# Kernel tuning notes

Measured on AMD Instinct MI355X. Metric: run time of the kernel, lower is better.

Reference implementation:

```python
import jax, jax.numpy as jnp
import numpy as np
from jax import lax

CODEBOOK_DIM = 32
SCALE_SCHEDULE = [1, 2, 4, 8, 16, 32, 64, 128, 256, 512, 1024, 2048, 4096, 8192]
INV_TEMP = 100.0
COMMIT_W = 0.2
ENTROPY_W = 0.1
EPS_NORM = 1e-12
EPS_LOG = 1e-8


def setup_inputs() -> dict:
    key = jax.random.key(0)
    B, T, C = 32, 8192, CODEBOOK_DIM
    f_BTC = jax.random.normal(key, (B, T, C), dtype=jnp.float32)
    return {"f_BTC": f_BTC}


def _area_down(x, pt):
    # torch F.interpolate mode='area' on divisible sizes == average pooling
    B, T, C = x.shape
    if pt == T:
        return x
    return x.reshape(B, pt, T // pt, C).mean(axis=2)


def _linear_up(x, out_size):
    # torch F.interpolate mode='linear', align_corners=False
    B, in_size, C = x.shape
    if out_size == in_size:
        return x
    scale = in_size / out_size
    pos = (jnp.arange(out_size, dtype=jnp.float32) + 0.5) * scale - 0.5
    pos = jnp.clip(pos, 0.0, in_size - 1)
    lo = jnp.floor(pos).astype(jnp.int32)
    hi = jnp.minimum(lo + 1, in_size - 1)
    w = (pos - lo.astype(jnp.float32))[None, :, None]
    return x[:, lo] * (1.0 - w) + x[:, hi] * w


def _bsq_level(z):
    # normalize
    norm = jnp.sqrt(jnp.sum(z * z, axis=-1, keepdims=True))
    z = z / jnp.maximum(norm, EPS_NORM)
    q_scale = 1.0 / (CODEBOOK_DIM ** 0.5)
    zhat = jnp.where(z > 0, q_scale, -q_scale).astype(z.dtype)
    quant = z + lax.stop_gradient(zhat - z)  # STE
    # soft entropy loss
    p = jax.nn.sigmoid(-4.0 * z / (CODEBOOK_DIM ** 0.5) * INV_TEMP)
    ent = lambda c: -(c * jnp.log(c + EPS_LOG))
    per_sample = (ent(p) + ent(1.0 - p)).sum(axis=-1).mean()
    avg_p = p.mean(axis=(0, 1))  # [C]
    cb_ent = (ent(avg_p) + ent(1.0 - avg_p)).sum()
    entropy_penalty = (per_sample - cb_ent) / INV_TEMP
    commit = jnp.mean(((lax.stop_gradient(quant) - z) ** 2).sum(axis=-1))
    aux = entropy_penalty * ENTROPY_W + commit * COMMIT_W
    bits = (quant > 0).astype(jnp.int32)
    return quant, bits, aux


def reference(f_BTC):
    B, T, C = f_BTC.shape
    quantized_out = jnp.zeros_like(f_BTC)
    residual = f_BTC
    all_losses, all_bits = [], []
    for pt in SCALE_SCHEDULE:
        r = _area_down(residual, pt)
        quant, bits, loss = _bsq_level(r)
        q_up = _linear_up(quant, T)
        residual = residual - lax.stop_gradient(q_up)
        quantized_out = quantized_out + q_up
        all_bits.append(bits)
        all_losses.append(loss)
    return quantized_out, jnp.concatenate(all_bits, axis=1), jnp.stack(all_losses, axis=-1)
```

## Files before the change

kernel.cpp:

```cpp
#include <hip/hip_runtime.h>

#define B_DIM 32
#define T_DIM 8192
#define C_DIM 32
#define N_ELEM (B_DIM * T_DIM * C_DIM)
#define SUM_PT 16383
#define BITS_ELEM (B_DIM * SUM_PT * C_DIM)
#define NLEVEL 14
#define PARTW 2048
#define QSCALE 0.17677669529663687f
#define ALPHA  70.710678118654755f

#define OWN 128
#define HALO 16
#define MAXL (OWN + 2 * HALO)

__device__ __forceinline__ float entf(float x) { return -(x * __logf(x + 1e-8f)); }
__device__ __forceinline__ float qval(float bit) { return bit * (2.0f * QSCALE) - QSCALE; }

__device__ __forceinline__ float interp_pk(const unsigned int* __restrict__ pkbase,
                                           int ptj, float tpos, int c) {
    const float a = (float)ptj * (1.0f / (float)T_DIM);
    float pos = (tpos + 0.5f) * a - 0.5f;
    pos = fminf(fmaxf(pos, 0.0f), (float)(ptj - 1));
    const int lo = (int)pos;
    const int hi = min(lo + 1, ptj - 1);
    const float w = pos - (float)lo;
    const float b0 = (float)((pkbase[lo] >> c) & 1u);
    const float b1 = (float)((pkbase[hi] >> c) & 1u);
    return ((b0 * (1.0f - w) + b1 * w) * 2.0f - 1.0f) * QSCALE;
}

template <int PTJ>
__device__ __forceinline__ float interp_loc(const unsigned int* __restrict__ bl,
                                            int p0, float tpos, int c) {
    const float a = (float)PTJ * (1.0f / (float)T_DIM);
    float pos = (tpos + 0.5f) * a - 0.5f;
    pos = fminf(fmaxf(pos, 0.0f), (float)(PTJ - 1));
    const int lo = (int)pos;
    const int hi = min(lo + 1, PTJ - 1);
    const float w = pos - (float)lo;
    const float b0 = (float)((bl[lo - p0] >> c) & 1u);
    const float b1 = (float)((bl[hi - p0] >> c) & 1u);
    return ((b0 * (1.0f - w) + b1 * w) * 2.0f - 1.0f) * QSCALE;
}

__device__ float pooled_up_sum64(const float* base, int ptj, int m) {
    const int W = 64;
    const float a = (float)ptj * (1.0f / (float)T_DIM);
    const float p0 = ((float)(m * W) + 0.5f) * a - 0.5f;
    const float pmax = (float)(ptj - 1);
    float sum = 0.0f;
    int iL = 0;
    if (p0 < 0.0f) { iL = (int)ceilf(-p0 / a); if (iL > W) iL = W; }
    int iH = W - 1;
    if (p0 + (float)(W - 1) * a > pmax) {
        iH = (int)floorf((pmax - p0) / a);
        if (iH > W - 1) iH = W - 1;
        if (iH < -1) iH = -1;
    }
    if (iL > 0) sum += (float)iL * qval(base[0]);
    if (iH < W - 1) sum += (float)(W - 1 - iH) * qval(base[(size_t)(ptj - 1) * C_DIM]);
    if (iH >= iL) {
        const float pL = p0 + (float)iL * a;
        int l0 = (int)pL;
        if (l0 > ptj - 1) l0 = ptj - 1;
        const int is = (int)ceilf(((float)(l0 + 1) - p0) / a);
        const int endA = min(is - 1, iH);
        if (endA >= iL) {
            const int nA = endA - iL + 1;
            const float sI = 0.5f * (float)(iL + endA) * (float)nA;
            const float SA = (float)nA * (p0 - (float)l0) + a * sI;
            const float q0 = qval(base[(size_t)l0 * C_DIM]);
            const float q1 = qval(base[(size_t)min(l0 + 1, ptj - 1) * C_DIM]);
            sum += (float)nA * q0 + SA * (q1 - q0);
        }
        const int begB = max(is, iL);
        if (begB <= iH) {
            const int nB = iH - begB + 1;
            const float sI = 0.5f * (float)(begB + iH) * (float)nB;
            const float SB = (float)nB * (p0 - (float)(l0 + 1)) + a * sI;
            const float q1 = qval(base[(size_t)min(l0 + 1, ptj - 1) * C_DIM]);
            const float q2 = qval(base[(size_t)min(l0 + 2, ptj - 1) * C_DIM]);
            sum += (float)nB * q1 + SB * (q2 - q1);
        }
    }
    return sum;
}

template <int NT>
__device__ __forceinline__ void write_partials(float eAcc, float cAcc, float pAcc,
                                               float* partial, int level, int col) {
    __shared__ float sP[NT];
    __shared__ float sEC[NT / 16];
    __syncthreads();
    const int grp = threadIdx.x >> 5, c = threadIdx.x & 31;
    float eg = eAcc, cg = cAcc;
#pragma unroll
    for (int m = 16; m >= 1; m >>= 1) { eg += __shfl_xor(eg, m, 32); cg += __shfl_xor(cg, m, 32); }
    if (c == 0) { sEC[grp * 2] = eg; sEC[grp * 2 + 1] = cg; }
    sP[threadIdx.x] = pAcc;
    __syncthreads();
    float* base = partial + (size_t)level * 34 * PARTW;
    if (threadIdx.x < 32) {
        float ps = 0.f;
#pragma unroll
        for (int r = 0; r < NT / 32; ++r) ps += sP[threadIdx.x + r * 32];
        base[(size_t)(2 + threadIdx.x) * PARTW + col] = ps;
    }
    if (threadIdx.x == 0) {
        float se = 0.f, sc = 0.f;
#pragma unroll
        for (int g = 0; g < NT / 32; ++g) { se += sEC[2 * g]; sc += sEC[2 * g + 1]; }
        base[0 * PARTW + col] = se;
        base[(size_t)1 * PARTW + col] = sc;
    }
}

__device__ __forceinline__ float bsq_eval(float v, float& bit, float& pA, float& eA, float& cA) {
    float sq = v * v;
#pragma unroll
    for (int m = 16; m >= 1; m >>= 1) sq += __shfl_xor(sq, m, 32);
    const float z = v / fmaxf(sqrtf(sq), 1e-12f);
    bit = (z > 0.f) ? 1.0f : 0.0f;
    const float zh = (z > 0.f) ? QSCALE : -QSCALE;
    const float d = zh - z;
    cA += d * d;
    const float p = 1.0f / (1.0f + __expf(ALPHA * z));
    pA += p;
    eA += entf(p) + entf(1.0f - p);
    return zh;
}

__global__ void init_kernel(const float* __restrict__ f, float* __restrict__ F128) {
    const int b = blockIdx.x >> 7, m = blockIdx.x & 127;
    const int c = threadIdx.x & 31, grp = threadIdx.x >> 5;
    const float* fb = f + ((size_t)b * T_DIM + m * 64 + grp * 8) * C_DIM + c;
    float s = 0.f;
#pragma unroll
    for (int i = 0; i < 8; ++i) s += fb[i * C_DIM];
    __shared__ float red[8][32];
    red[grp][c] = s;
    __syncthreads();
    if (grp == 0) {
        float t = red[0][c] + red[1][c] + red[2][c] + red[3][c]
                + red[4][c] + red[5][c] + red[6][c] + red[7][c];
        F128[((size_t)b * 128 + m) * C_DIM + c] = t * (1.0f / 64.0f);
    }
}

__global__ __launch_bounds__(1024) void fused_small_kernel(const float* __restrict__ F128,
                                                           float* __restrict__ bits,
                                                           unsigned int* __restrict__ pkG,
                                                           float* __restrict__ partial) {
    const int b = blockIdx.x;
    __shared__ float P[128 * 32];
    __shared__ float qh[127 * 32];
    const int c = threadIdx.x & 31, grp = threadIdx.x >> 5;
    for (int i = threadIdx.x; i < 128 * 32; i += 1024) P[i] = F128[(size_t)b * 128 * 32 + i];
    __syncthreads();
    for (int k = 0; k < 8; ++k) {
        const int pt = 1 << k, W2 = 128 >> k;
        float pAcc = 0.f, eAcc = 0.f, cAcc = 0.f;
        for (int o = grp; o < pt; o += 32) {
            float v = 0.f;
            for (int i = 0; i < W2; ++i) v += P[(o * W2 + i) * 32 + c];
            v *= (1.0f / (float)W2);
            float bit;
            bsq_eval(v, bit, pAcc, eAcc, cAcc);
            bits[((size_t)b * SUM_PT + (pt - 1) + o) * C_DIM + c] = bit;
            const unsigned long long bal = __ballot(bit > 0.5f);
            if (c == 0)
                pkG[(size_t)b * 256 + (pt - 1) + o] =
                    (threadIdx.x & 32) ? (unsigned)(bal >> 32) : (unsigned)bal;
            if (k < 7) qh[((pt - 1) + o) * 32 + c] = bit;
        }
        write_partials<1024>(eAcc, cAcc, pAcc, partial, k, b);
        if (k < 7) {
            __syncthreads();
            for (int m = grp; m < 128; m += 32)
                P[m * 32 + c] -= pooled_up_sum64(&qh[(pt - 1) * 32 + c], 1 << k, m) * (1.0f / 64.0f);
            __syncthreads();
        }
    }
}

template <int K, int OFF>
__device__ __forceinline__ void cf_level(float* Rl, unsigned int* bitsPyr,
                                         const float* wT, const int* iT,
                                         float* __restrict__ bits,
                                         float* __restrict__ partial, int b,
                                         int L0, int nL, int r0, int r1,
                                         int c, int grp) {
    constexpr int F = 4096 >> K;
    constexpr int ptk = 1 << K;
    const int p0 = L0 / F, pN = nL / F;
    const int own0 = r0 / F, own1 = r1 / F;
    unsigned int* bl = bitsPyr + OFF;
    float pAcc = 0.f, eAcc = 0.f, cAcc = 0.f;
    for (int pl = grp; pl < pN; pl += 16) {
        float v = 0.f;
#pragma unroll
        for (int r = 0; r < F; ++r) v += Rl[(pl * F + r) * 32 + c];
        v *= (1.0f / (float)F);
        float sq = v * v;
#pragma unroll
        for (int m = 16; m >= 1; m >>= 1) sq += __shfl_xor(sq, m, 32);
        const float z = v / fmaxf(sqrtf(sq), 1e-12f);
        const unsigned long long bal = __ballot(z > 0.f);
        const unsigned int word = (threadIdx.x & 32) ? (unsigned)(bal >> 32) : (unsigned)bal;
        if (c == 0) bl[pl] = word;
        const int mg = p0 + pl;
        if (mg >= own0 && mg < own1) {
            bits[((size_t)b * SUM_PT + (ptk - 1) + mg) * C_DIM + c] = (z > 0.f) ? 1.f : 0.f;
            const float zh = (z > 0.f) ? QSCALE : -QSCALE;
            const float d = zh - z;
            cAcc += d * d;
            const float p = 1.0f / (1.0f + __expf(ALPHA * z));
            pAcc += p;
            eAcc += entf(p) + entf(1.0f - p);
        }
    }
    write_partials<512>(eAcc, cAcc, pAcc, partial, K, blockIdx.x);
    if (K < 12) {
        for (int rl = grp; rl < nL; rl += 16) {
            const float w = wT[rl];
            const int pk = iT[rl];
            const float b0 = (float)((bl[pk & 0xFFFF] >> c) & 1u);
            const float b1 = (float)((bl[pk >> 16] >> c) & 1u);
            Rl[rl * 32 + c] -= ((b0 * (1.0f - w) + b1 * w) * 2.0f - 1.0f) * QSCALE;
        }
        __syncthreads();
    }
}

__global__ __launch_bounds__(512) void chunk_final_kernel(const float* __restrict__ f,
                                                          float* __restrict__ outQ,
                                                          float* __restrict__ bits,
                                                          const unsigned int* __restrict__ pkG,
                                                          float* __restrict__ partial) {
    const int b = blockIdx.x >> 5;
    const int chunk = blockIdx.x & 31;
    const int r0 = chunk * OWN, r1 = r0 + OWN;
    const int L0 = max(0, r0 - HALO);
    const int L1 = min(4096, r1 + HALO);
    const int nL = L1 - L0;
    const int nSeg = nL >> 4;
    __shared__ float Rl[MAXL * 32];
    __shared__ unsigned int bitsPyr[310];
    __shared__ unsigned int pk07[255];
    __shared__ float segA[16][32], segB[16][32];
    __shared__ float wT[4 * MAXL];
    __shared__ int iT[4 * MAXL];
    const int c = threadIdx.x & 31, grp = threadIdx.x >> 5;

    const float* fb = f + ((size_t)b * T_DIM + (size_t)L0 * 2) * C_DIM;
    for (int i = threadIdx.x; i < nL * 8; i += 512) {
        const int row = i >> 3, c4 = i & 7;
        const float4 v0 = *(const float4*)(fb + (size_t)(2 * row) * 32 + c4 * 4);
        const float4 v1 = *(const float4*)(fb + (size_t)(2 * row + 1) * 32 + c4 * 4);
        float4 o;
        o.x = 0.5f * (v0.x + v1.x); o.y = 0.5f * (v0.y + v1.y);
        o.z = 0.5f * (v0.z + v1.z); o.w = 0.5f * (v0.w + v1.w);
        *(float4*)(Rl + row * 32 + c4 * 4) = o;
    }
    for (int i = threadIdx.x; i < 255; i += 512) pk07[i] = pkG[(size_t)b * 256 + i];
    for (int idx = threadIdx.x; idx < 4 * nL; idx += 512) {
        const int lvl = idx / nL, rl = idx - lvl * nL;
        const int ptk = 256 << lvl;
        const int F = 4096 / ptk;
        const int p0 = L0 / F, pN = nL / F;
        const float a = (float)ptk * (1.0f / (float)T_DIM);
        float pos = (float)(2 * (L0 + rl) + 1) * a - 0.5f;
        pos = fminf(fmaxf(pos, 0.0f), (float)(ptk - 1));
        const int lo = (int)pos;
        const int hi = min(lo + 1, ptk - 1);
        wT[idx] = pos - (float)lo;
        const int lol = min(max(lo - p0, 0), pN - 1);
        const int hil = min(max(hi - p0, 0), pN - 1);
        iT[idx] = lol | (hil << 16);
    }
    __syncthreads();

    for (int w = threadIdx.x; w < nSeg * 32; w += 512) {
        const int s = w >> 5, cc = w & 31;
        const int rg = L0 + s * 16;
        float c0 = 0.f, c1 = 0.f;
#pragma unroll
        for (int j = 0; j < 8; ++j) {
            const int ptj = 1 << j;
            c0 += interp_pk(pk07 + (ptj - 1), ptj, (float)(2 * rg) + 0.5f, cc);
            c1 += interp_pk(pk07 + (ptj - 1), ptj, (float)(2 * rg + 2) + 0.5f, cc);
        }
        segA[s][cc] = c0;
        segB[s][cc] = c1 - c0;
    }
    __syncthreads();
    for (int rl = grp; rl < nL; rl += 16) {
        const int s = rl >> 4;
        Rl[rl * 32 + c] -= fmaf((float)(rl & 15), segB[s][c], segA[s][c]);
    }
    __syncthreads();

    cf_level<8, 0>(Rl, bitsPyr, wT + 0 * nL, iT + 0 * nL, bits, partial, b, L0, nL, r0, r1, c, grp);
    cf_level<9, 10>(Rl, bitsPyr, wT + 1 * nL, iT + 1 * nL, bits, partial, b, L0, nL, r0, r1, c, grp);
    cf_level<10, 30>(Rl, bitsPyr, wT + 2 * nL, iT + 2 * nL, bits, partial, b, L0, nL, r0, r1, c, grp);
    cf_level<11, 70>(Rl, bitsPyr, wT + 3 * nL, iT + 3 * nL, bits, partial, b, L0, nL, r0, r1, c, grp);
    cf_level<12, 150>(Rl, bitsPyr, wT, iT, bits, partial, b, L0, nL, r0, r1, c, grp);

    __syncthreads();
    const int t0 = 2 * r0;
    const int p8 = L0 / 16, p9 = L0 / 8, p10 = L0 / 4, p11 = L0 / 2;
    for (int w = threadIdx.x; w < 16 * 32; w += 512) {
        const int s = w >> 5, cc = w & 31;
        const int tA = t0 + s * 16;
        float c0 = 0.f, c1 = 0.f;
#pragma unroll
        for (int j = 0; j < 8; ++j) {
            const int ptj = 1 << j;
            c0 += interp_pk(pk07 + (ptj - 1), ptj, (float)tA, cc);
            c1 += interp_pk(pk07 + (ptj - 1), ptj, (float)(tA + 1), cc);
        }
        c0 += interp_loc<256>(bitsPyr + 0, p8, (float)tA, cc);
        c1 += interp_loc<256>(bitsPyr + 0, p8, (float)(tA + 1), cc);
        segA[s][cc] = c0;
        segB[s][cc] = c1 - c0;
    }
    __syncthreads();
    const unsigned int* bl9 = bitsPyr + 10;
    const unsigned int* bl10 = bitsPyr + 30;
    const unsigned int* bl11 = bitsPyr + 70;
    const unsigned int* bl12 = bitsPyr + 150;
    float pAcc = 0.f, eAcc = 0.f, cAcc = 0.f;
    for (int j2 = grp; j2 < OWN; j2 += 16) {
        const int mg = r0 + j2;
        const int lr = mg - L0;
        const int te = 2 * mg;
        const int tte = 2 * j2;
        const int s = tte >> 4;

        const int e9 = te & 15;
        int lo9 = (te >> 4) - 1 + (e9 >= 8 ? 1 : 0);
        float w9e = (e9 < 8 ? (float)(17 + 2 * e9) : (float)(2 * e9 - 15)) * (1.0f / 32.0f);
        float w9o = w9e + (1.0f / 16.0f);
        if (lo9 < 0) { lo9 = 0; w9e = 0.f; w9o = 0.f; }
        const int hi9 = min(lo9 + 1, 511);
        const float b9a = (float)((bl9[lo9 - p9] >> c) & 1u);
        const float b9b = (float)((bl9[hi9 - p9] >> c) & 1u);

        const int e10 = te & 7;
        int lo10 = (te >> 3) - 1 + (e10 >= 4 ? 1 : 0);
        float w10e = (e10 < 4 ? (float)(9 + 2 * e10) : (float)(2 * e10 - 7)) * (1.0f / 16.0f);
        float w10o = w10e + (1.0f / 8.0f);
        if (lo10 < 0) { lo10 = 0; w10e = 0.f; w10o = 0.f; }
        const int hi10 = min(lo10 + 1, 1023);
        const float b10a = (float)((bl10[lo10 - p10] >> c) & 1u);
        const float b10b = (float)((bl10[hi10 - p10] >> c) & 1u);

        const int e11 = te & 3;
        int lo11 = (te >> 2) - 1 + (e11 >= 2 ? 1 : 0);
        float w11e = (e11 < 2 ? (float)(5 + 2 * e11) : (float)(2 * e11 - 3)) * (1.0f / 8.0f);
        float w11o = w11e + (1.0f / 4.0f);
        if (lo11 < 0) { lo11 = 0; w11e = 0.f; w11o = 0.f; }
        const int hi11 = min(lo11 + 1, 2047);
        const float b11a = (float)((bl11[lo11 - p11] >> c) & 1u);
        const float b11b = (float)((bl11[hi11 - p11] >> c) & 1u);

        const float q12m1 = (float)((bl12[max(lr - 1, 0)] >> c) & 1u);
        const float q12z = (float)((bl12[lr] >> c) & 1u);
        const float q12p1 = (float)((bl12[min(lr + 1, nL - 1)] >> c) & 1u);
        const float w12e = (mg == 0) ? 0.f : 0.75f;
        const float w12o = 0.25f;

        float upe = fmaf((float)(tte & 15), segB[s][c], segA[s][c]);
        upe += ((b9a * (1.0f - w9e) + b9b * w9e) * 2.0f - 1.0f) * QSCALE;
        upe += ((b10a * (1.0f - w10e) + b10b * w10e) * 2.0f - 1.0f) * QSCALE;
        upe += ((b11a * (1.0f - w11e) + b11b * w11e) * 2.0f - 1.0f) * QSCALE;
        upe += ((q12m1 * (1.0f - w12e) + q12z * w12e) * 2.0f - 1.0f) * QSCALE;

        float upo = fmaf((float)((tte + 1) & 15), segB[s][c], segA[s][c]);
        upo += ((b9a * (1.0f - w9o) + b9b * w9o) * 2.0f - 1.0f) * QSCALE;
        upo += ((b10a * (1.0f - w10o) + b10b * w10o) * 2.0f - 1.0f) * QSCALE;
        upo += ((b11a * (1.0f - w11o) + b11b * w11o) * 2.0f - 1.0f) * QSCALE;
        upo += ((q12z * (1.0f - w12o) + q12p1 * w12o) * 2.0f - 1.0f) * QSCALE;

        {
            const size_t idx = ((size_t)b * T_DIM + te) * C_DIM + c;
            const float v = f[idx] - upe;
            float bit;
            const float zh = bsq_eval(v, bit, pAcc, eAcc, cAcc);
            bits[((size_t)b * SUM_PT + (T_DIM - 1) + te) * C_DIM + c] = bit;
            outQ[idx] = upe + zh;
        }
        {
            const size_t idx = ((size_t)b * T_DIM + te + 1) * C_DIM + c;
            const float v = f[idx] - upo;
            float bit;
            const float zh = bsq_eval(v, bit, pAcc, eAcc, cAcc);
            bits[((size_t)b * SUM_PT + (T_DIM - 1) + te + 1) * C_DIM + c] = bit;
            outQ[idx] = upo + zh;
        }
    }
    write_partials<512>(eAcc, cAcc, pAcc, partial, 13, blockIdx.x);
}

__global__ __launch_bounds__(1024) void reduce_finalize(const float* __restrict__ partial,
                                                        float* __restrict__ outL) {
    __shared__ float accS[NLEVEL * 34];
    const int tid = threadIdx.x;
    if (tid < NLEVEL * 34) {
        const int level = tid / 34, comp = tid % 34;
        const int nblk = (level < 8) ? 32 : 1024;
        const float* s = partial + ((size_t)level * 34 + comp) * PARTW;
        float v0 = 0.f, v1 = 0.f, v2 = 0.f, v3 = 0.f;
        for (int i = 0; i < nblk; i += 4) {
            v0 += s[i]; v1 += s[i + 1]; v2 += s[i + 2]; v3 += s[i + 3];
        }
        accS[tid] = (v0 + v1) + (v2 + v3);
    }
    __syncthreads();
    const int k = tid >> 5, c = tid & 31;
    if (k < NLEVEL) {
        const float cnt = (float)(B_DIM << k);
        const float avg_p = accS[k * 34 + 2 + c] / cnt;
        float ec = entf(avg_p) + entf(1.0f - avg_p);
#pragma unroll
        for (int m = 16; m >= 1; m >>= 1) ec += __shfl_xor(ec, m, 32);
        if (c == 0) {
            const float per_sample = accS[k * 34 + 0] / cnt;
            const float commit = accS[k * 34 + 1] / cnt;
            const float pen = (per_sample - ec) * (1.0f / 100.0f);
            outL[k] = pen * 0.1f + commit * 0.2f;
        }
    }
}

extern "C" void kernel_launch(void* const* d_in, const int* in_sizes, int n_in,
                              void* d_out, int out_size, void* d_ws, size_t ws_size,
                              hipStream_t stream) {
    (void)in_sizes; (void)n_in; (void)out_size; (void)ws_size;
    const float* f = (const float*)d_in[0];
    float* outQ = (float*)d_out;
    float* outBits = outQ + N_ELEM;
    float* outL = outBits + BITS_ELEM;

    float* partial = (float*)d_ws;
    float* acc = partial + (size_t)NLEVEL * 34 * PARTW;
    float* F128 = acc + NLEVEL * 64;
    unsigned int* pkG = (unsigned int*)(F128 + (size_t)B_DIM * 128 * C_DIM);

    init_kernel<<<B_DIM * 128, 256, 0, stream>>>(f, F128);
    fused_small_kernel<<<B_DIM, 1024, 0, stream>>>(F128, outBits, pkG, partial);
    chunk_final_kernel<<<B_DIM * 32, 512, 0, stream>>>(f, outQ, outBits, pkG, partial);
    reduce_finalize<<<1, 1024, 0, stream>>>(partial, outL);
}
```

Baseline: 182.7 us.

## Replace block partial reductions with per-wave writes and stop updating residual in LDS

Block-level partial reductions, each with two __syncthreads, are replaced by per-wavefront shuffle reductions that write straight to a larger partials buffer. The final reduction is split into a wide multi-block reduce kernel and a tiny finalize kernel. The chunk kernel no longer subtracts each level's upsampled quantization from the LDS residual rows. Instead it subtracts the contributions of earlier coarse levels at pooled positions, using precomputed interpolation tables. This cuts per-row LDS read-modify-write passes and barriers, but adds an extra kernel launch and more partial data to reduce.

```diff
diff --git a/kernel.cpp b/kernel.cpp
--- a/kernel.cpp
+++ b/kernel.cpp
@@ -7,7 +7,8 @@
 #define SUM_PT 16383
 #define BITS_ELEM (B_DIM * SUM_PT * C_DIM)
 #define NLEVEL 14
-#define PARTW 2048
+#define PARTB 8192
+#define PARTS 512
 #define QSCALE 0.17677669529663687f
 #define ALPHA  70.710678118654755f
 
@@ -42,6 +43,13 @@
     const float w = pos - (float)lo;
     const float b0 = (float)((bl[lo - p0] >> c) & 1u);
     const float b1 = (float)((bl[hi - p0] >> c) & 1u);
+    return ((b0 * (1.0f - w) + b1 * w) * 2.0f - 1.0f) * QSCALE;
+}
+
+__device__ __forceinline__ float evalT(const unsigned int* __restrict__ bl,
+                                       float w, int pk, int c) {
+    const float b0 = (float)((bl[pk & 0xFFFF] >> c) & 1u);
+    const float b1 = (float)((bl[pk >> 16] >> c) & 1u);
     return ((b0 * (1.0f - w) + b1 * w) * 2.0f - 1.0f) * QSCALE;
 }
 
@@ -88,33 +96,15 @@
     return sum;
 }
 
-template <int NT>
-__device__ __forceinline__ void write_partials(float eAcc, float cAcc, float pAcc,
-                                               float* partial, int level, int col) {
-    __shared__ float sP[NT];
-    __shared__ float sEC[NT / 16];
-    __syncthreads();
-    const int grp = threadIdx.x >> 5, c = threadIdx.x & 31;
-    float eg = eAcc, cg = cAcc;
-#pragma unroll
-    for (int m = 16; m >= 1; m >>= 1) { eg += __shfl_xor(eg, m, 32); cg += __shfl_xor(cg, m, 32); }
-    if (c == 0) { sEC[grp * 2] = eg; sEC[grp * 2 + 1] = cg; }
-    sP[threadIdx.x] = pAcc;
-    __syncthreads();
-    float* base = partial + (size_t)level * 34 * PARTW;
-    if (threadIdx.x < 32) {
-        float ps = 0.f;
-#pragma unroll
-        for (int r = 0; r < NT / 32; ++r) ps += sP[threadIdx.x + r * 32];
-        base[(size_t)(2 + threadIdx.x) * PARTW + col] = ps;
-    }
-    if (threadIdx.x == 0) {
-        float se = 0.f, sc = 0.f;
-#pragma unroll
-        for (int g = 0; g < NT / 32; ++g) { se += sEC[2 * g]; sc += sEC[2 * g + 1]; }
-        base[0 * PARTW + col] = se;
-        base[(size_t)1 * PARTW + col] = sc;
-    }
+__device__ __forceinline__ void wave_partials(float e, float cm, float p,
+                                              float* base, int stride, int col) {
+    float eg = e, cg = cm;
+#pragma unroll
+    for (int m = 32; m >= 1; m >>= 1) { eg += __shfl_xor(eg, m, 64); cg += __shfl_xor(cg, m, 64); }
+    const float p2 = p + __shfl_xor(p, 32, 64);
+    const int lane = threadIdx.x & 63;
+    if (lane < 32) base[(size_t)(2 + lane) * stride + col] = p2;
+    if (lane == 0) { base[col] = eg; base[(size_t)stride + col] = cg; }
 }
 
 __device__ __forceinline__ float bsq_eval(float v, float& bit, float& pA, float& eA, float& cA) {
@@ -152,11 +142,12 @@
 __global__ __launch_bounds__(1024) void fused_small_kernel(const float* __restrict__ F128,
                                                            float* __restrict__ bits,
                                                            unsigned int* __restrict__ pkG,
-                                                           float* __restrict__ partial) {
+                                                           float* __restrict__ pSm) {
     const int b = blockIdx.x;
     __shared__ float P[128 * 32];
     __shared__ float qh[127 * 32];
     const int c = threadIdx.x & 31, grp = threadIdx.x >> 5;
+    const int col = b * 16 + (threadIdx.x >> 6);
     for (int i = threadIdx.x; i < 128 * 32; i += 1024) P[i] = F128[(size_t)b * 128 * 32 + i];
     __syncthreads();
     for (int k = 0; k < 8; ++k) {
@@ -175,7 +166,7 @@
                     (threadIdx.x & 32) ? (unsigned)(bal >> 32) : (unsigned)bal;
             if (k < 7) qh[((pt - 1) + o) * 32 + c] = bit;
         }
-        write_partials<1024>(eAcc, cAcc, pAcc, partial, k, b);
+        wave_partials(eAcc, cAcc, pAcc, pSm + (size_t)k * 34 * PARTS, PARTS, col);
         if (k < 7) {
             __syncthreads();
             for (int m = grp; m < 128; m += 32)
@@ -185,15 +176,42 @@
     }
 }
 
-template <int K, int OFF>
-__device__ __forceinline__ void cf_level(float* Rl, unsigned int* bitsPyr,
-                                         const float* wT, const int* iT,
+template <int K, int J, int TO>
+__device__ __forceinline__ void buildTab(float* tw, int* ti, int L0, int nL) {
+    constexpr int FK = 4096 >> K;
+    constexpr int ptj = 1 << J;
+    constexpr int FJ = 4096 >> J;
+    const int pN = nL / FK;
+    const int p0j = L0 / FJ;
+    const int pNj = nL / FJ;
+    for (int pl = threadIdx.x; pl < pN; pl += 512) {
+        const float tpos = (float)(2 * (L0 + pl * FK) + FK) - 0.5f;
+        const float a = (float)ptj * (1.0f / (float)T_DIM);
+        float pos = (tpos + 0.5f) * a - 0.5f;
+        pos = fminf(fmaxf(pos, 0.0f), (float)(ptj - 1));
+        const int lo = (int)pos;
+        const int hi = min(lo + 1, ptj - 1);
+        tw[TO + pl] = pos - (float)lo;
+        const int lol = min(max(lo - p0j, 0), pNj - 1);
+        const int hil = min(max(hi - p0j, 0), pNj - 1);
+        ti[TO + pl] = lol | (hil << 16);
+    }
+}
+
+template <int K>
+__device__ __forceinline__ void cf_level(const float* Rl, unsigned int* bitsPyr,
+                                         const float* tw, const int* ti,
                                          float* __restrict__ bits,
-                                         float* __restrict__ partial, int b,
-                                         int L0, int nL, int r0, int r1,
-                                         int c, int grp) {
+                                         float* __restrict__ pBig,
+                                         int b, int L0, int nL, int r0, int r1,
+                                         int c, int grp, int col) {
     constexpr int F = 4096 >> K;
     constexpr int ptk = 1 << K;
+    constexpr int OFF = (K == 8) ? 0 : (K == 9) ? 10 : (K == 10) ? 30 : (K == 11) ? 70 : 150;
+    constexpr int TB8 = (K == 9) ? 0 : (K == 10) ? 20 : (K == 11) ? 100 : 340;
+    constexpr int TB9 = (K == 10) ? 60 : (K == 11) ? 180 : 500;
+    constexpr int TB10 = (K == 11) ? 260 : 660;
+    constexpr int TB11 = 820;
     const int p0 = L0 / F, pN = nL / F;
     const int own0 = r0 / F, own1 = r1 / F;
     unsigned int* bl = bitsPyr + OFF;
@@ -203,6 +221,10 @@
 #pragma unroll
         for (int r = 0; r < F; ++r) v += Rl[(pl * F + r) * 32 + c];
         v *= (1.0f / (float)F);
+        if (K >= 9)  v -= evalT(bitsPyr + 0,  tw[TB8 + pl],  ti[TB8 + pl], c);
+        if (K >= 10) v -= evalT(bitsPyr + 10, tw[TB9 + pl],  ti[TB9 + pl], c);
+        if (K >= 11) v -= evalT(bitsPyr + 30, tw[TB10 + pl], ti[TB10 + pl], c);
+        if (K >= 12) v -= evalT(bitsPyr + 70, tw[TB11 + pl], ti[TB11 + pl], c);
         float sq = v * v;
 #pragma unroll
         for (int m = 16; m >= 1; m >>= 1) sq += __shfl_xor(sq, m, 32);
@@ -221,24 +243,15 @@
             eAcc += entf(p) + entf(1.0f - p);
         }
     }
-    write_partials<512>(eAcc, cAcc, pAcc, partial, K, blockIdx.x);
-    if (K < 12) {
-        for (int rl = grp; rl < nL; rl += 16) {
-            const float w = wT[rl];
-            const int pk = iT[rl];
-            const float b0 = (float)((bl[pk & 0xFFFF] >> c) & 1u);
-            const float b1 = (float)((bl[pk >> 16] >> c) & 1u);
-            Rl[rl * 32 + c] -= ((b0 * (1.0f - w) + b1 * w) * 2.0f - 1.0f) * QSCALE;
-        }
-        __syncthreads();
-    }
+    wave_partials(eAcc, cAcc, pAcc, pBig + (size_t)(K - 8) * 34 * PARTB, PARTB, col);
+    __syncthreads();
 }
 
 __global__ __launch_bounds__(512) void chunk_final_kernel(const float* __restrict__ f,
                                                           float* __restrict__ outQ,
                                                           float* __restrict__ bits,
                                                           const unsigned int* __restrict__ pkG,
-                                                          float* __restrict__ partial) {
+                                                          float* __restrict__ pBig) {
     const int b = blockIdx.x >> 5;
     const int chunk = blockIdx.x & 31;
     const int r0 = chunk * OWN, r1 = r0 + OWN;
@@ -250,9 +263,10 @@
     __shared__ unsigned int bitsPyr[310];
     __shared__ unsigned int pk07[255];
     __shared__ float segA[16][32], segB[16][32];
-    __shared__ float wT[4 * MAXL];
-    __shared__ int iT[4 * MAXL];
+    __shared__ float tw[980];
+    __shared__ int ti[980];
     const int c = threadIdx.x & 31, grp = threadIdx.x >> 5;
+    const int col = blockIdx.x * 8 + (threadIdx.x >> 6);
 
     const float* fb = f + ((size_t)b * T_DIM + (size_t)L0 * 2) * C_DIM;
     for (int i = threadIdx.x; i < nL * 8; i += 512) {
@@ -265,21 +279,16 @@
         *(float4*)(Rl + row * 32 + c4 * 4) = o;
     }
     for (int i = threadIdx.x; i < 255; i += 512) pk07[i] = pkG[(size_t)b * 256 + i];
-    for (int idx = threadIdx.x; idx < 4 * nL; idx += 512) {
-        const int lvl = idx / nL, rl = idx - lvl * nL;
-        const int ptk = 256 << lvl;
-        const int F = 4096 / ptk;
-        const int p0 = L0 / F, pN = nL / F;
-        const float a = (float)ptk * (1.0f / (float)T_DIM);
-        float pos = (float)(2 * (L0 + rl) + 1) * a - 0.5f;
-        pos = fminf(fmaxf(pos, 0.0f), (float)(ptk - 1));
-        const int lo = (int)pos;
-        const int hi = min(lo + 1, ptk - 1);
-        wT[idx] = pos - (float)lo;
-        const int lol = min(max(lo - p0, 0), pN - 1);
-        const int hil = min(max(hi - p0, 0), pN - 1);
-        iT[idx] = lol | (hil << 16);
-    }
+    buildTab<9, 8, 0>(tw, ti, L0, nL);
+    buildTab<10, 8, 20>(tw, ti, L0, nL);
+    buildTab<10, 9, 60>(tw, ti, L0, nL);
+    buildTab<11, 8, 100>(tw, ti, L0, nL);
+    buildTab<11, 9, 180>(tw, ti, L0, nL);
+    buildTab<11, 10, 260>(tw, ti, L0, nL);
+    buildTab<12, 8, 340>(tw, ti, L0, nL);
+    buildTab<12, 9, 500>(tw, ti, L0, nL);
+    buildTab<12, 10, 660>(tw, ti, L0, nL);
+    buildTab<12, 11, 820>(tw, ti, L0, nL);
     __syncthreads();
 
     for (int w = threadIdx.x; w < nSeg * 32; w += 512) {
@@ -302,13 +311,12 @@
     }
     __syncthreads();
 
-    cf_level<8, 0>(Rl, bitsPyr, wT + 0 * nL, iT + 0 * nL, bits, partial, b, L0, nL, r0, r1, c, grp);
-    cf_level<9, 10>(Rl, bitsPyr, wT + 1 * nL, iT + 1 * nL, bits, partial, b, L0, nL, r0, r1, c, grp);
-    cf_level<10, 30>(Rl, bitsPyr, wT + 2 * nL, iT + 2 * nL, bits, partial, b, L0, nL, r0, r1, c, grp);
-    cf_level<11, 70>(Rl, bitsPyr, wT + 3 * nL, iT + 3 * nL, bits, partial, b, L0, nL, r0, r1, c, grp);
-    cf_level<12, 150>(Rl, bitsPyr, wT, iT, bits, partial, b, L0, nL, r0, r1, c, grp);
-
-    __syncthreads();
+    cf_level<8>(Rl, bitsPyr, tw, ti, bits, pBig, b, L0, nL, r0, r1, c, grp, col);
+    cf_level<9>(Rl, bitsPyr, tw, ti, bits, pBig, b, L0, nL, r0, r1, c, grp, col);
+    cf_level<10>(Rl, bitsPyr, tw, ti, bits, pBig, b, L0, nL, r0, r1, c, grp, col);
+    cf_level<11>(Rl, bitsPyr, tw, ti, bits, pBig, b, L0, nL, r0, r1, c, grp, col);
+    cf_level<12>(Rl, bitsPyr, tw, ti, bits, pBig, b, L0, nL, r0, r1, c, grp, col);
+
     const int t0 = 2 * r0;
     const int p8 = L0 / 16, p9 = L0 / 8, p10 = L0 / 4, p11 = L0 / 2;
     for (int w = threadIdx.x; w < 16 * 32; w += 512) {
@@ -401,37 +409,39 @@
             outQ[idx] = upo + zh;
         }
     }
-    write_partials<512>(eAcc, cAcc, pAcc, partial, 13, blockIdx.x);
-}
-
-__global__ __launch_bounds__(1024) void reduce_finalize(const float* __restrict__ partial,
-                                                        float* __restrict__ outL) {
-    __shared__ float accS[NLEVEL * 34];
-    const int tid = threadIdx.x;
-    if (tid < NLEVEL * 34) {
-        const int level = tid / 34, comp = tid % 34;
-        const int nblk = (level < 8) ? 32 : 1024;
-        const float* s = partial + ((size_t)level * 34 + comp) * PARTW;
-        float v0 = 0.f, v1 = 0.f, v2 = 0.f, v3 = 0.f;
-        for (int i = 0; i < nblk; i += 4) {
-            v0 += s[i]; v1 += s[i + 1]; v2 += s[i + 2]; v3 += s[i + 3];
-        }
-        accS[tid] = (v0 + v1) + (v2 + v3);
-    }
-    __syncthreads();
-    const int k = tid >> 5, c = tid & 31;
-    if (k < NLEVEL) {
-        const float cnt = (float)(B_DIM << k);
-        const float avg_p = accS[k * 34 + 2 + c] / cnt;
-        float ec = entf(avg_p) + entf(1.0f - avg_p);
-#pragma unroll
-        for (int m = 16; m >= 1; m >>= 1) ec += __shfl_xor(ec, m, 32);
-        if (c == 0) {
-            const float per_sample = accS[k * 34 + 0] / cnt;
-            const float commit = accS[k * 34 + 1] / cnt;
-            const float pen = (per_sample - ec) * (1.0f / 100.0f);
-            outL[k] = pen * 0.1f + commit * 0.2f;
-        }
+    wave_partials(eAcc, cAcc, pAcc, pBig + (size_t)5 * 34 * PARTB, PARTB, col);
+}
+
+__global__ void reduce_partials(const float* __restrict__ pSm,
+                                const float* __restrict__ pBig,
+                                float* __restrict__ acc) {
+    const int level = blockIdx.x / 34;
+    const int comp = blockIdx.x % 34;
+    const float* s;
+    int n;
+    if (level < 8) { s = pSm + ((size_t)level * 34 + comp) * PARTS; n = PARTS; }
+    else { s = pBig + ((size_t)(level - 8) * 34 + comp) * PARTB; n = PARTB; }
+    float v = 0.f;
+    for (int i = threadIdx.x; i < n; i += 64) v += s[i];
+#pragma unroll
+    for (int m = 32; m >= 1; m >>= 1) v += __shfl_xor(v, m, 64);
+    if (threadIdx.x == 0) acc[level * 34 + comp] = v;
+}
+
+__global__ void finalize_kernel(const float* __restrict__ acc, float* __restrict__ outL) {
+    const int k = threadIdx.x >> 5;
+    const int c = threadIdx.x & 31;
+    if (k >= NLEVEL) return;
+    const float cnt = (float)(B_DIM << k);
+    const float avg_p = acc[k * 34 + 2 + c] / cnt;
+    float ec = entf(avg_p) + entf(1.0f - avg_p);
+#pragma unroll
+    for (int m = 16; m >= 1; m >>= 1) ec += __shfl_xor(ec, m, 32);
+    if (c == 0) {
+        const float per_sample = acc[k * 34 + 0] / cnt;
+        const float commit = acc[k * 34 + 1] / cnt;
+        const float pen = (per_sample - ec) * (1.0f / 100.0f);
+        outL[k] = pen * 0.1f + commit * 0.2f;
     }
 }
 
@@ -444,13 +454,15 @@
     float* outBits = outQ + N_ELEM;
     float* outL = outBits + BITS_ELEM;
 
-    float* partial = (float*)d_ws;
-    float* acc = partial + (size_t)NLEVEL * 34 * PARTW;
-    float* F128 = acc + NLEVEL * 64;
+    float* pSm = (float*)d_ws;
+    float* pBig = pSm + (size_t)8 * 34 * PARTS;
+    float* acc = pBig + (size_t)6 * 34 * PARTB;
+    float* F128 = acc + NLEVEL * 34;
     unsigned int* pkG = (unsigned int*)(F128 + (size_t)B_DIM * 128 * C_DIM);
 
     init_kernel<<<B_DIM * 128, 256, 0, stream>>>(f, F128);
-    fused_small_kernel<<<B_DIM, 1024, 0, stream>>>(F128, outBits, pkG, partial);
-    chunk_final_kernel<<<B_DIM * 32, 512, 0, stream>>>(f, outQ, outBits, pkG, partial);
-    reduce_finalize<<<1, 1024, 0, stream>>>(partial, outL);
-}
+    fused_small_kernel<<<B_DIM, 1024, 0, stream>>>(F128, outBits, pkG, pSm);
+    chunk_final_kernel<<<B_DIM * 32, 512, 0, stream>>>(f, outQ, outBits, pkG, pBig);
+    reduce_partials<<<NLEVEL * 34, 64, 0, stream>>>(pSm, pBig, acc);
+    finalize_kernel<<<1, 512, 0, stream>>>(acc, outL);
+}
```

Result: faster. 173.9 us (-4.8%).
